# Performance work log

Hardware: AMD Instinct MI355X
Metric: run time of the kernel (lower is better)

The kernel has to match this reference:

```python
import jax, jax.numpy as jnp
import numpy as np

B, N, DIM = 4, 2048, 1024
HEADS, DHEAD = 16, 64
N_MEM = 64
INNER = HEADS * DHEAD  # 1024


def setup_inputs() -> dict:
    key = jax.random.key(0)
    ks = jax.random.split(key, 8)
    x = jax.random.normal(ks[0], (B, N, DIM), dtype=jnp.float32)
    memories = jax.random.normal(ks[1], (N_MEM, DIM), dtype=jnp.float32)
    attn_mask = jnp.ones((1, 1, N, N + N_MEM), dtype=bool)
    scale = 1.0 / np.sqrt(DIM)
    ln_gamma = jnp.ones((DIM,), dtype=jnp.float32)
    ln_beta = jnp.zeros((DIM,), dtype=jnp.float32)
    Wq = jax.random.normal(ks[2], (DIM, INNER), dtype=jnp.float32) * scale
    Wkv = jax.random.normal(ks[3], (DIM, 2 * INNER), dtype=jnp.float32) * scale
    Wo = jax.random.normal(ks[4], (INNER, DIM), dtype=jnp.float32) * scale
    bo = jnp.zeros((DIM,), dtype=jnp.float32)
    return {"x": x, "attn_mask": attn_mask, "memories": memories,
            "ln_gamma": ln_gamma, "ln_beta": ln_beta,
            "Wq": Wq, "Wkv": Wkv, "Wo": Wo, "bo": bo}


def _layernorm(x, gamma, beta, eps=1e-5):
    mu = jnp.mean(x, axis=-1, keepdims=True)
    var = jnp.var(x, axis=-1, keepdims=True)
    return (x - mu) * jax.lax.rsqrt(var + eps) * gamma + beta


def reference(x, attn_mask, memories, ln_gamma, ln_beta, Wq, Wkv, Wo, bo):
    b = x.shape[0]
    xn = _layernorm(x, ln_gamma, ln_beta)
    # memories: [n_mem, d] -> broadcast to [b, n_mem, d], concat on kv length
    mem = jnp.broadcast_to(memories[None], (b, memories.shape[0], memories.shape[1]))
    x_kv = jnp.concatenate([xn, mem], axis=1)  # [b, n+n_mem, d]
    q = xn @ Wq                                 # [b, n, inner]
    kv = x_kv @ Wkv                             # [b, nk, 2*inner]
    k, v = jnp.split(kv, 2, axis=-1)
    # split heads: b n (h d) -> b h n d
    def heads(t):
        bsz, n, _ = t.shape
        return t.reshape(bsz, n, HEADS, DHEAD).transpose(0, 2, 1, 3)
    q, k, v = heads(q), heads(k), heads(v)
    scale = DHEAD ** -0.5
    dots = jnp.einsum('bhnd,bhmd->bhnm', q, k) * scale  # [b,h,n,nk]
    neg = -jnp.finfo(dots.dtype).max
    dots = jnp.where(attn_mask, dots, neg)
    attn = jax.nn.softmax(dots, axis=-1)
    out = jnp.einsum('bhnm,bhmd->bhnd', attn, v)        # [b,h,n,d]
    out = out.transpose(0, 2, 1, 3).reshape(b, -1, INNER)
    return out @ Wo + bo
```

## Files before the change

kernel.cpp:

```cpp
#include <hip/hip_runtime.h>

using f16 = _Float16;
typedef _Float16 f16x8 __attribute__((ext_vector_type(8)));
typedef _Float16 f16x4 __attribute__((ext_vector_type(4)));
typedef float f32x4 __attribute__((ext_vector_type(4)));
typedef float f32x16 __attribute__((ext_vector_type(16)));
typedef uint32_t u32;
typedef unsigned int u32x4 __attribute__((ext_vector_type(4)));
typedef __fp16 h16x2 __attribute__((ext_vector_type(2)));

constexpr int DIMC   = 1024;
constexpr int NSEQ   = 2048;
constexpr int NKV    = 2112;
constexpr int NCHUNK = 33;
constexpr int NBATCH = 4;

__device__ __forceinline__ int swz8(int row, int slot) { return slot ^ (row & 7); }

__device__ __forceinline__ u32 pkrtz(float a, float b) {
    h16x2 t = __builtin_amdgcn_cvt_pkrtz(a, b);
    return __builtin_bit_cast(u32, t);
}

__device__ __forceinline__ void gld16(const f16* g, f16* l) {
    __builtin_amdgcn_global_load_lds(
        (const __attribute__((address_space(1))) u32*)g,
        (__attribute__((address_space(3))) u32*)l,
        16, 0, 0);
}

__global__ __launch_bounds__(256)
void ln_kernel(const float* __restrict__ x, const float* __restrict__ gamma,
               const float* __restrict__ beta, f16* __restrict__ xn)
{
    const int row = blockIdx.x;
    const int tid = threadIdx.x;
    const float4 v = *reinterpret_cast<const float4*>(x + (size_t)row * DIMC + tid * 4);
    float s  = v.x + v.y + v.z + v.w;
    float ss = v.x*v.x + v.y*v.y + v.z*v.z + v.w*v.w;
#pragma unroll
    for (int off = 1; off < 64; off <<= 1) {
        s  += __shfl_xor(s,  off, 64);
        ss += __shfl_xor(ss, off, 64);
    }
    __shared__ float ps[4], pss[4];
    const int w = tid >> 6;
    if ((tid & 63) == 0) { ps[w] = s; pss[w] = ss; }
    __syncthreads();
    s  = ps[0]  + ps[1]  + ps[2]  + ps[3];
    ss = pss[0] + pss[1] + pss[2] + pss[3];
    const float mu   = s * (1.0f / 1024.0f);
    const float var  = ss * (1.0f / 1024.0f) - mu * mu;
    const float rstd = rsqrtf(var + 1e-5f);
    const float4 gv = *reinterpret_cast<const float4*>(gamma + tid * 4);
    const float4 bv = *reinterpret_cast<const float4*>(beta  + tid * 4);
    f16x4 o;
    o[0] = (f16)((v.x - mu) * rstd * gv.x + bv.x);
    o[1] = (f16)((v.y - mu) * rstd * gv.y + bv.y);
    o[2] = (f16)((v.z - mu) * rstd * gv.z + bv.z);
    o[3] = (f16)((v.w - mu) * rstd * gv.w + bv.w);
    *reinterpret_cast<f16x4*>(xn + (size_t)row * DIMC + tid * 4) = o;
}

__global__ __launch_bounds__(256)
void transpose_cast(const float* __restrict__ in, f16* __restrict__ out,
                    int R, int C, float scale)
{
    __shared__ float tile[32][33];
    const int c0 = blockIdx.x * 32;
    const int r0 = blockIdx.y * 32;
    const int tx = threadIdx.x;
    const int ty = threadIdx.y;
#pragma unroll
    for (int i = 0; i < 4; ++i)
        tile[ty + i * 8][tx] = in[(size_t)(r0 + ty + i * 8) * C + c0 + tx];
    __syncthreads();
#pragma unroll
    for (int i = 0; i < 4; ++i)
        out[(size_t)(c0 + ty + i * 8) * R + r0 + tx] = (f16)(tile[tx][ty + i * 8] * scale);
}

__global__ __launch_bounds__(256)
void cast_kernel(const float* __restrict__ in, f16* __restrict__ out)
{
    const int i = blockIdx.x * 256 + threadIdx.x;
    const float4 v = *reinterpret_cast<const float4*>(in + (size_t)i * 4);
    f16x4 o; o[0] = (f16)v.x; o[1] = (f16)v.y; o[2] = (f16)v.z; o[3] = (f16)v.w;
    *reinterpret_cast<f16x4*>(out + (size_t)i * 4) = o;
}

template<int MODE>
__device__ __forceinline__ void gemm_body(
    int tm, int tn, f16* As, f16* Bs,
    const f16* __restrict__ A, const f16* __restrict__ BT,
    const f16* __restrict__ mem16,
    f16* __restrict__ Cf16, f16* __restrict__ Vt,
    float* __restrict__ Cf32, const float* __restrict__ bias)
{
    const int tid = threadIdx.x;
    const int lane = tid & 63, w = tid >> 6;
    const int wm = (w >> 1) * 64, wn = (w & 1) * 64;
    const int l3 = lane >> 3, l7 = lane & 7;
    const int gslot = (l7 ^ l3) * 8;

    f32x4 acc[4][4] = {};

    const f16* ag[4];
    const f16* bg[4];
#pragma unroll
    for (int i = 0; i < 4; ++i) {
        const int rl = w * 32 + i * 8 + l3;
        const int gm = tm * 128 + rl;
        if (MODE == 1) {
            const int bb = gm / NKV;
            const int rr = gm - bb * NKV;
            ag[i] = ((rr < NSEQ) ? (A + ((size_t)bb * NSEQ + rr) * DIMC)
                                 : (mem16 + (size_t)(rr - NSEQ) * DIMC)) + gslot;
        } else {
            ag[i] = A + (size_t)gm * DIMC + gslot;
        }
        bg[i] = BT + (size_t)(tn * 128 + rl) * DIMC + gslot;
    }

    for (int kt = 0; kt < DIMC; kt += 64) {
#pragma unroll
        for (int i = 0; i < 4; ++i) {
            gld16(ag[i] + kt, &As[(w * 32 + i * 8) * 64]);
            gld16(bg[i] + kt, &Bs[(w * 32 + i * 8) * 64]);
        }
        asm volatile("s_waitcnt vmcnt(0)" ::: "memory");
        __syncthreads();
#pragma unroll
        for (int kk = 0; kk < 2; ++kk) {
            f16x8 af[4], bf[4];
            const int rsel  = lane & 15;
            const int slot0 = (lane >> 4) + kk * 4;
#pragma unroll
            for (int mi = 0; mi < 4; ++mi) {
                const int row = wm + mi * 16 + rsel;
                af[mi] = *reinterpret_cast<const f16x8*>(&As[row * 64 + swz8(row, slot0) * 8]);
            }
#pragma unroll
            for (int nj = 0; nj < 4; ++nj) {
                const int row = wn + nj * 16 + rsel;
                bf[nj] = *reinterpret_cast<const f16x8*>(&Bs[row * 64 + swz8(row, slot0) * 8]);
            }
            __builtin_amdgcn_s_setprio(1);
#pragma unroll
            for (int mi = 0; mi < 4; ++mi)
#pragma unroll
                for (int nj = 0; nj < 4; ++nj)
                    acc[mi][nj] = __builtin_amdgcn_mfma_f32_16x16x32_f16(af[mi], bf[nj], acc[mi][nj], 0, 0, 0);
            __builtin_amdgcn_s_setprio(0);
        }
        __syncthreads();
    }

    const int cl = lane & 15, g = lane >> 4;
#pragma unroll
    for (int mi = 0; mi < 4; ++mi) {
#pragma unroll
        for (int nj = 0; nj < 4; ++nj) {
            const int col = tn * 128 + wn + nj * 16 + cl;
            if (MODE == 1 && col >= DIMC) {
                const int gm0 = tm * 128 + wm + mi * 16 + g * 4;
                const int bb = gm0 / NKV;
                const int rr = gm0 - bb * NKV;
                const int vc = col - DIMC;
                f16x4 pk;
                pk[0] = (f16)acc[mi][nj][0]; pk[1] = (f16)acc[mi][nj][1];
                pk[2] = (f16)acc[mi][nj][2]; pk[3] = (f16)acc[mi][nj][3];
                *reinterpret_cast<f16x4*>(
                    Vt + ((((size_t)bb * 16 + (vc >> 6)) * NCHUNK + (rr >> 6)) * 64 + (vc & 63)) * 64 + (rr & 63)) = pk;
            } else {
#pragma unroll
                for (int j = 0; j < 4; ++j) {
                    const int gm = tm * 128 + wm + mi * 16 + g * 4 + j;
                    const float val = acc[mi][nj][j];
                    if (MODE == 0) {
                        const int bb = gm >> 11, rr = gm & 2047;
                        Cf16[(((size_t)bb * 16 + (col >> 6)) * NSEQ + rr) * 64 + (col & 63)] = (f16)val;
                    } else if (MODE == 1) {
                        const int bb = gm / NKV;
                        const int rr = gm - bb * NKV;
                        Cf16[(((size_t)bb * 16 + (col >> 6)) * NKV + rr) * 64 + (col & 63)] = (f16)val;
                    } else {
                        Cf32[(size_t)gm * DIMC + col] = val + bias[col];
                    }
                }
            }
        }
    }
}

__global__ __launch_bounds__(256, 3)
void gemm_qkv(const f16* __restrict__ xn, const f16* __restrict__ wqT,
              const f16* __restrict__ wkvT, const f16* __restrict__ mem16,
              f16* __restrict__ q16, f16* __restrict__ k16, f16* __restrict__ vt16)
{
    __shared__ __align__(16) f16 As[128 * 64];
    __shared__ __align__(16) f16 Bs[128 * 64];
    if (blockIdx.y < 16) {
        gemm_body<1>(blockIdx.x, blockIdx.y, As, Bs, xn, wkvT, mem16, k16, vt16, nullptr, nullptr);
    } else {
        if (blockIdx.x >= 64) return;
        gemm_body<0>(blockIdx.x, blockIdx.y - 16, As, Bs, xn, wqT, nullptr, q16, nullptr, nullptr, nullptr);
    }
}

__global__ __launch_bounds__(256, 3)
void gemm_o(const f16* __restrict__ ao, const f16* __restrict__ woT,
            float* __restrict__ out, const float* __restrict__ bo)
{
    __shared__ __align__(16) f16 As[128 * 64];
    __shared__ __align__(16) f16 Bs[128 * 64];
    gemm_body<2>(blockIdx.x, blockIdx.y, As, Bs, ao, woT, nullptr, nullptr, nullptr, out, bo);
}

__global__ __launch_bounds__(256, 2)
void attn_kernel(const f16* __restrict__ q16, const f16* __restrict__ k16,
                 const f16* __restrict__ vt16, f16* __restrict__ ao16)
{
    __shared__ __align__(16) f16 Kb[4][64 * 64];
    __shared__ __align__(16) f16 Vb[4][64 * 64];

    const int raw = blockIdx.x;
    const int bh = (raw & 7) * 8 + ((raw >> 3) & 7);
    const int qt = raw >> 6;
    const int b = bh >> 4, h = bh & 15;
    const int tid = threadIdx.x, lane = tid & 63, w = tid >> 6;
    const int l31 = lane & 31, hi = lane >> 5;
    const int l3 = lane >> 3, l7 = lane & 7;
    const int gslot = (l7 ^ l3) * 8;

    const f16* kbase = k16  + (size_t)bh * NKV * 64;
    const f16* vbase = vt16 + (size_t)bh * NCHUNK * 4096;
    const f16* qbase = q16  + (size_t)bh * NSEQ * 64;

    const f16* kp[2];
    const f16* vp[2];
#pragma unroll
    for (int i = 0; i < 2; ++i) {
        const int off = (w * 16 + i * 8 + l3) * 64 + gslot;
        kp[i] = kbase + off;
        vp[i] = vbase + off;
    }

    f16x8 qf[2][4];
#pragma unroll
    for (int qb = 0; qb < 2; ++qb)
#pragma unroll
        for (int ks = 0; ks < 4; ++ks) {
            const int qrow = qt * 256 + w * 64 + qb * 32 + l31;
            qf[qb][ks] = *reinterpret_cast<const f16x8*>(
                qbase + (size_t)qrow * 64 + ks * 16 + hi * 8);
        }

    f32x16 Oa[2][2] = {};
    float lacc[2] = {0.0f, 0.0f};

#pragma unroll
    for (int c = 0; c < 3; ++c) {
#pragma unroll
        for (int i = 0; i < 2; ++i) {
            gld16(kp[i] + (size_t)c * 4096, &Kb[c][(w * 16 + i * 8) * 64]);
            gld16(vp[i] + (size_t)c * 4096, &Vb[c][(w * 16 + i * 8) * 64]);
        }
    }

    for (int t = 0; t < NCHUNK; ++t) {
        if (t <= 30)      asm volatile("s_waitcnt vmcnt(8)" ::: "memory");
        else if (t == 31) asm volatile("s_waitcnt vmcnt(4)" ::: "memory");
        else              asm volatile("s_waitcnt vmcnt(0)" ::: "memory");
        __builtin_amdgcn_s_barrier();

        if (t <= 29) {
            const int nb = (t + 3) & 3;
#pragma unroll
            for (int i = 0; i < 2; ++i) {
                gld16(kp[i] + (size_t)(t + 3) * 4096, &Kb[nb][(w * 16 + i * 8) * 64]);
                gld16(vp[i] + (size_t)(t + 3) * 4096, &Vb[nb][(w * 16 + i * 8) * 64]);
            }
        }
        const f16* Ks = Kb[t & 3];
        const f16* Vs = Vb[t & 3];

#pragma unroll
        for (int kb = 0; kb < 2; ++kb) {
            const int krow = kb * 32 + l31;
            f16x8 kf[4];
#pragma unroll
            for (int ks = 0; ks < 4; ++ks)
                kf[ks] = *reinterpret_cast<const f16x8*>(
                    &Ks[krow * 64 + ((2 * ks + hi) ^ (krow & 7)) * 8]);

            f32x16 sA = {}, sB = {};
            __builtin_amdgcn_s_setprio(1);
#pragma unroll
            for (int ks = 0; ks < 4; ++ks) {
                sA = __builtin_amdgcn_mfma_f32_32x32x16_f16(kf[ks], qf[0][ks], sA, 0, 0, 0);
                sB = __builtin_amdgcn_mfma_f32_32x32x16_f16(kf[ks], qf[1][ks], sB, 0, 0, 0);
            }
            __builtin_amdgcn_s_setprio(0);

            f16x8 pb[2][2];
#pragma unroll
            for (int qb = 0; qb < 2; ++qb) {
                const f32x16 sv = qb ? sB : sA;
                float p[16];
                float sum = 0.0f;
#pragma unroll
                for (int r = 0; r < 16; ++r) {
                    p[r] = __builtin_amdgcn_exp2f(sv[r] - 8.0f);
                    sum += p[r];
                }
                lacc[qb] += sum;
#pragma unroll
                for (int s2 = 0; s2 < 2; ++s2) {
                    u32 a  = pkrtz(p[s2 * 8 + 0], p[s2 * 8 + 1]);
                    u32 bb2 = pkrtz(p[s2 * 8 + 2], p[s2 * 8 + 3]);
                    u32 c  = pkrtz(p[s2 * 8 + 4], p[s2 * 8 + 5]);
                    u32 d  = pkrtz(p[s2 * 8 + 6], p[s2 * 8 + 7]);
                    asm volatile("v_permlane32_swap_b32 %0, %1" : "+v"(a),  "+v"(c));
                    asm volatile("v_permlane32_swap_b32 %0, %1" : "+v"(bb2), "+v"(d));
                    u32x4 wv = {a, bb2, c, d};
                    pb[qb][s2] = __builtin_bit_cast(f16x8, wv);
                }
            }

#pragma unroll
            for (int s2 = 0; s2 < 2; ++s2) {
                const int s = kb * 2 + s2;
                const int vr1 = 32 + l31;
                const f16x8 vf0 = *reinterpret_cast<const f16x8*>(
                    &Vs[l31 * 64 + ((2 * s + hi) ^ (l31 & 7)) * 8]);
                const f16x8 vf1 = *reinterpret_cast<const f16x8*>(
                    &Vs[vr1 * 64 + ((2 * s + hi) ^ (vr1 & 7)) * 8]);
                __builtin_amdgcn_s_setprio(1);
                Oa[0][0] = __builtin_amdgcn_mfma_f32_32x32x16_f16(vf0, pb[0][s2], Oa[0][0], 0, 0, 0);
                Oa[0][1] = __builtin_amdgcn_mfma_f32_32x32x16_f16(vf1, pb[0][s2], Oa[0][1], 0, 0, 0);
                Oa[1][0] = __builtin_amdgcn_mfma_f32_32x32x16_f16(vf0, pb[1][s2], Oa[1][0], 0, 0, 0);
                Oa[1][1] = __builtin_amdgcn_mfma_f32_32x32x16_f16(vf1, pb[1][s2], Oa[1][1], 0, 0, 0);
                __builtin_amdgcn_s_setprio(0);
            }
        }
        __builtin_amdgcn_s_barrier();
    }

#pragma unroll
    for (int qb = 0; qb < 2; ++qb) {
        const float l0 = lacc[qb] + __shfl_xor(lacc[qb], 32, 64);
        const float rinv = 1.0f / l0;
        const int qrow = qt * 256 + w * 64 + qb * 32 + l31;
#pragma unroll
        for (int db = 0; db < 2; ++db) {
#pragma unroll
            for (int rq = 0; rq < 4; ++rq) {
                const int d0 = db * 32 + rq * 8 + hi * 4;
                f16x4 pk;
                pk[0] = (f16)(Oa[qb][db][rq * 4 + 0] * rinv);
                pk[1] = (f16)(Oa[qb][db][rq * 4 + 1] * rinv);
                pk[2] = (f16)(Oa[qb][db][rq * 4 + 2] * rinv);
                pk[3] = (f16)(Oa[qb][db][rq * 4 + 3] * rinv);
                *reinterpret_cast<f16x4*>(
                    ao16 + ((size_t)(b * NSEQ + qrow)) * DIMC + h * 64 + d0) = pk;
            }
        }
    }
}

extern "C" void kernel_launch(void* const* d_in, const int* in_sizes, int n_in,
                              void* d_out, int out_size, void* d_ws, size_t ws_size,
                              hipStream_t stream)
{
    const float* x        = (const float*)d_in[0];
    const float* memories = (const float*)d_in[2];
    const float* ln_gamma = (const float*)d_in[3];
    const float* ln_beta  = (const float*)d_in[4];
    const float* Wq       = (const float*)d_in[5];
    const float* Wkv      = (const float*)d_in[6];
    const float* Wo       = (const float*)d_in[7];
    const float* bo       = (const float*)d_in[8];
    float* out = (float*)d_out;

    char* ws = (char*)d_ws;
    f16* xn16  = (f16*)(ws);
    f16* q16   = (f16*)(ws + (16ull << 20));
    f16* k16   = (f16*)(ws + (32ull << 20));
    f16* vt16  = (f16*)(ws + (49ull << 20));
    f16* wqT   = (f16*)(ws + (66ull << 20));
    f16* wkvT  = (f16*)(ws + (68ull << 20));
    f16* woT   = (f16*)(ws + (72ull << 20));
    f16* mem16 = (f16*)(ws + (74ull << 20));
    f16* ao16  = xn16;

    transpose_cast<<<dim3(32, 32), dim3(32, 8), 0, stream>>>(Wq,  wqT,  1024, 1024, 0.125f * 1.44269504088896341f);
    transpose_cast<<<dim3(64, 32), dim3(32, 8), 0, stream>>>(Wkv, wkvT, 1024, 2048, 1.0f);
    transpose_cast<<<dim3(32, 32), dim3(32, 8), 0, stream>>>(Wo,  woT,  1024, 1024, 1.0f);
    cast_kernel<<<64, 256, 0, stream>>>(memories, mem16);

    ln_kernel<<<NBATCH * NSEQ, 256, 0, stream>>>(x, ln_gamma, ln_beta, xn16);

    gemm_qkv<<<dim3(66, 24), 256, 0, stream>>>(xn16, wqT, wkvT, mem16, q16, k16, vt16);

    attn_kernel<<<dim3(512), 256, 0, stream>>>(q16, k16, vt16, ao16);

    gemm_o<<<dim3(64, 8), 256, 0, stream>>>(ao16, woT, out, bo);

    (void)in_sizes; (void)n_in; (void)out_size; (void)ws_size;
}
```

Baseline: 216.8 us.

## Split attention work across 8 waves with double-buffered K/V and fdot2 row sums

The attention kernel moves from 4 waves each owning 64 query rows to 8 waves each owning 32 rows, which halves per-wave accumulators and raises occupancy through launch bounds of 512 threads. The K/V LDS ring shrinks from a 4-deep prefetch to a 2-deep double buffer with a full vmcnt(0) wait every chunk. Row-sum accumulation now uses packed fp16 dot products on the already-rounded probabilities instead of fp32 adds. The trade is more latency hiding from extra waves against a shallower prefetch, less K fragment reuse per wave, and a softmax sum taken from fp16-rounded values.

```diff
diff --git a/kernel.cpp b/kernel.cpp
--- a/kernel.cpp
+++ b/kernel.cpp
@@ -217,12 +217,12 @@
     gemm_body<2>(blockIdx.x, blockIdx.y, As, Bs, ao, woT, nullptr, nullptr, nullptr, out, bo);
 }
 
-__global__ __launch_bounds__(256, 2)
+__global__ __launch_bounds__(512, 4)
 void attn_kernel(const f16* __restrict__ q16, const f16* __restrict__ k16,
                  const f16* __restrict__ vt16, f16* __restrict__ ao16)
 {
-    __shared__ __align__(16) f16 Kb[4][64 * 64];
-    __shared__ __align__(16) f16 Vb[4][64 * 64];
+    __shared__ __align__(16) f16 Kb[2][64 * 64];
+    __shared__ __align__(16) f16 Vb[2][64 * 64];
 
     const int raw = blockIdx.x;
     const int bh = (raw & 7) * 8 + ((raw >> 3) & 7);
@@ -237,53 +237,38 @@
     const f16* vbase = vt16 + (size_t)bh * NCHUNK * 4096;
     const f16* qbase = q16  + (size_t)bh * NSEQ * 64;
 
-    const f16* kp[2];
-    const f16* vp[2];
-#pragma unroll
-    for (int i = 0; i < 2; ++i) {
-        const int off = (w * 16 + i * 8 + l3) * 64 + gslot;
-        kp[i] = kbase + off;
-        vp[i] = vbase + off;
-    }
-
-    f16x8 qf[2][4];
-#pragma unroll
-    for (int qb = 0; qb < 2; ++qb)
-#pragma unroll
-        for (int ks = 0; ks < 4; ++ks) {
-            const int qrow = qt * 256 + w * 64 + qb * 32 + l31;
-            qf[qb][ks] = *reinterpret_cast<const f16x8*>(
+    const int srow = w * 8 + l3;
+    const f16* kp = kbase + (size_t)srow * 64 + gslot;
+    const f16* vp = vbase + (size_t)srow * 64 + gslot;
+
+    f16x8 qf[4];
+    {
+        const int qrow = qt * 256 + w * 32 + l31;
+#pragma unroll
+        for (int ks = 0; ks < 4; ++ks)
+            qf[ks] = *reinterpret_cast<const f16x8*>(
                 qbase + (size_t)qrow * 64 + ks * 16 + hi * 8);
-        }
-
-    f32x16 Oa[2][2] = {};
-    float lacc[2] = {0.0f, 0.0f};
-
-#pragma unroll
-    for (int c = 0; c < 3; ++c) {
-#pragma unroll
-        for (int i = 0; i < 2; ++i) {
-            gld16(kp[i] + (size_t)c * 4096, &Kb[c][(w * 16 + i * 8) * 64]);
-            gld16(vp[i] + (size_t)c * 4096, &Vb[c][(w * 16 + i * 8) * 64]);
-        }
-    }
+    }
+
+    f32x16 Oa0 = {}, Oa1 = {};
+    float lp0 = 0.0f, lp1 = 0.0f, lp2 = 0.0f, lp3 = 0.0f;
+
+    gld16(kp, &Kb[0][w * 8 * 64]);
+    gld16(vp, &Vb[0][w * 8 * 64]);
+
+#if __has_builtin(__builtin_amdgcn_fdot2)
+    const h16x2 ones = {(__fp16)1.0f, (__fp16)1.0f};
+#endif
 
     for (int t = 0; t < NCHUNK; ++t) {
-        if (t <= 30)      asm volatile("s_waitcnt vmcnt(8)" ::: "memory");
-        else if (t == 31) asm volatile("s_waitcnt vmcnt(4)" ::: "memory");
-        else              asm volatile("s_waitcnt vmcnt(0)" ::: "memory");
+        asm volatile("s_waitcnt vmcnt(0)" ::: "memory");
         __builtin_amdgcn_s_barrier();
-
-        if (t <= 29) {
-            const int nb = (t + 3) & 3;
-#pragma unroll
-            for (int i = 0; i < 2; ++i) {
-                gld16(kp[i] + (size_t)(t + 3) * 4096, &Kb[nb][(w * 16 + i * 8) * 64]);
-                gld16(vp[i] + (size_t)(t + 3) * 4096, &Vb[nb][(w * 16 + i * 8) * 64]);
-            }
-        }
-        const f16* Ks = Kb[t & 3];
-        const f16* Vs = Vb[t & 3];
+        if (t + 1 < NCHUNK) {
+            gld16(kp + (size_t)(t + 1) * 4096, &Kb[(t + 1) & 1][w * 8 * 64]);
+            gld16(vp + (size_t)(t + 1) * 4096, &Vb[(t + 1) & 1][w * 8 * 64]);
+        }
+        const f16* Ks = Kb[t & 1];
+        const f16* Vs = Vb[t & 1];
 
 #pragma unroll
         for (int kb = 0; kb < 2; ++kb) {
@@ -294,38 +279,44 @@
                 kf[ks] = *reinterpret_cast<const f16x8*>(
                     &Ks[krow * 64 + ((2 * ks + hi) ^ (krow & 7)) * 8]);
 
-            f32x16 sA = {}, sB = {};
+            f32x16 sA = {};
             __builtin_amdgcn_s_setprio(1);
 #pragma unroll
-            for (int ks = 0; ks < 4; ++ks) {
-                sA = __builtin_amdgcn_mfma_f32_32x32x16_f16(kf[ks], qf[0][ks], sA, 0, 0, 0);
-                sB = __builtin_amdgcn_mfma_f32_32x32x16_f16(kf[ks], qf[1][ks], sB, 0, 0, 0);
-            }
+            for (int ks = 0; ks < 4; ++ks)
+                sA = __builtin_amdgcn_mfma_f32_32x32x16_f16(kf[ks], qf[ks], sA, 0, 0, 0);
             __builtin_amdgcn_s_setprio(0);
 
-            f16x8 pb[2][2];
-#pragma unroll
-            for (int qb = 0; qb < 2; ++qb) {
-                const f32x16 sv = qb ? sB : sA;
-                float p[16];
-                float sum = 0.0f;
-#pragma unroll
-                for (int r = 0; r < 16; ++r) {
-                    p[r] = __builtin_amdgcn_exp2f(sv[r] - 8.0f);
-                    sum += p[r];
+            float p[16];
+#pragma unroll
+            for (int r = 0; r < 16; ++r)
+                p[r] = __builtin_amdgcn_exp2f(sA[r] - 8.0f);
+
+            f16x8 pb[2];
+#pragma unroll
+            for (int s2 = 0; s2 < 2; ++s2) {
+                u32 a  = pkrtz(p[s2 * 8 + 0], p[s2 * 8 + 1]);
+                u32 b2 = pkrtz(p[s2 * 8 + 2], p[s2 * 8 + 3]);
+                u32 c  = pkrtz(p[s2 * 8 + 4], p[s2 * 8 + 5]);
+                u32 d  = pkrtz(p[s2 * 8 + 6], p[s2 * 8 + 7]);
+                asm volatile("v_permlane32_swap_b32 %0, %1" : "+v"(a),  "+v"(c));
+                asm volatile("v_permlane32_swap_b32 %0, %1" : "+v"(b2), "+v"(d));
+#if __has_builtin(__builtin_amdgcn_fdot2)
+                lp0 = __builtin_amdgcn_fdot2(__builtin_bit_cast(h16x2, a),  ones, lp0, false);
+                lp1 = __builtin_amdgcn_fdot2(__builtin_bit_cast(h16x2, b2), ones, lp1, false);
+                lp2 = __builtin_amdgcn_fdot2(__builtin_bit_cast(h16x2, c),  ones, lp2, false);
+                lp3 = __builtin_amdgcn_fdot2(__builtin_bit_cast(h16x2, d),  ones, lp3, false);
+#else
+                {
+                    h16x2 ha = __builtin_bit_cast(h16x2, a),  hb = __builtin_bit_cast(h16x2, b2);
+                    h16x2 hc = __builtin_bit_cast(h16x2, c),  hd = __builtin_bit_cast(h16x2, d);
+                    lp0 += (float)ha[0] + (float)ha[1];
+                    lp1 += (float)hb[0] + (float)hb[1];
+                    lp2 += (float)hc[0] + (float)hc[1];
+                    lp3 += (float)hd[0] + (float)hd[1];
                 }
-                lacc[qb] += sum;
-#pragma unroll
-                for (int s2 = 0; s2 < 2; ++s2) {
-                    u32 a  = pkrtz(p[s2 * 8 + 0], p[s2 * 8 + 1]);
-                    u32 bb2 = pkrtz(p[s2 * 8 + 2], p[s2 * 8 + 3]);
-                    u32 c  = pkrtz(p[s2 * 8 + 4], p[s2 * 8 + 5]);
-                    u32 d  = pkrtz(p[s2 * 8 + 6], p[s2 * 8 + 7]);
-                    asm volatile("v_permlane32_swap_b32 %0, %1" : "+v"(a),  "+v"(c));
-                    asm volatile("v_permlane32_swap_b32 %0, %1" : "+v"(bb2), "+v"(d));
-                    u32x4 wv = {a, bb2, c, d};
-                    pb[qb][s2] = __builtin_bit_cast(f16x8, wv);
-                }
+#endif
+                u32x4 wv = {a, b2, c, d};
+                pb[s2] = __builtin_bit_cast(f16x8, wv);
             }
 
 #pragma unroll
@@ -337,35 +328,38 @@
                 const f16x8 vf1 = *reinterpret_cast<const f16x8*>(
                     &Vs[vr1 * 64 + ((2 * s + hi) ^ (vr1 & 7)) * 8]);
                 __builtin_amdgcn_s_setprio(1);
-                Oa[0][0] = __builtin_amdgcn_mfma_f32_32x32x16_f16(vf0, pb[0][s2], Oa[0][0], 0, 0, 0);
-                Oa[0][1] = __builtin_amdgcn_mfma_f32_32x32x16_f16(vf1, pb[0][s2], Oa[0][1], 0, 0, 0);
-                Oa[1][0] = __builtin_amdgcn_mfma_f32_32x32x16_f16(vf0, pb[1][s2], Oa[1][0], 0, 0, 0);
-                Oa[1][1] = __builtin_amdgcn_mfma_f32_32x32x16_f16(vf1, pb[1][s2], Oa[1][1], 0, 0, 0);
+                Oa0 = __builtin_amdgcn_mfma_f32_32x32x16_f16(vf0, pb[s2], Oa0, 0, 0, 0);
+                Oa1 = __builtin_amdgcn_mfma_f32_32x32x16_f16(vf1, pb[s2], Oa1, 0, 0, 0);
                 __builtin_amdgcn_s_setprio(0);
             }
         }
-        __builtin_amdgcn_s_barrier();
-    }
-
-#pragma unroll
-    for (int qb = 0; qb < 2; ++qb) {
-        const float l0 = lacc[qb] + __shfl_xor(lacc[qb], 32, 64);
-        const float rinv = 1.0f / l0;
-        const int qrow = qt * 256 + w * 64 + qb * 32 + l31;
-#pragma unroll
-        for (int db = 0; db < 2; ++db) {
-#pragma unroll
-            for (int rq = 0; rq < 4; ++rq) {
-                const int d0 = db * 32 + rq * 8 + hi * 4;
-                f16x4 pk;
-                pk[0] = (f16)(Oa[qb][db][rq * 4 + 0] * rinv);
-                pk[1] = (f16)(Oa[qb][db][rq * 4 + 1] * rinv);
-                pk[2] = (f16)(Oa[qb][db][rq * 4 + 2] * rinv);
-                pk[3] = (f16)(Oa[qb][db][rq * 4 + 3] * rinv);
-                *reinterpret_cast<f16x4*>(
-                    ao16 + ((size_t)(b * NSEQ + qrow)) * DIMC + h * 64 + d0) = pk;
-            }
-        }
+    }
+
+    float l0 = (lp0 + lp1) + (lp2 + lp3);
+    l0 += __shfl_xor(l0, 32, 64);
+    const float rinv = 1.0f / l0;
+    const int qrow = qt * 256 + w * 32 + l31;
+#pragma unroll
+    for (int rq = 0; rq < 4; ++rq) {
+        const int d0 = rq * 8 + hi * 4;
+        f16x4 pk;
+        pk[0] = (f16)(Oa0[rq * 4 + 0] * rinv);
+        pk[1] = (f16)(Oa0[rq * 4 + 1] * rinv);
+        pk[2] = (f16)(Oa0[rq * 4 + 2] * rinv);
+        pk[3] = (f16)(Oa0[rq * 4 + 3] * rinv);
+        *reinterpret_cast<f16x4*>(
+            ao16 + ((size_t)(b * NSEQ + qrow)) * DIMC + h * 64 + d0) = pk;
+    }
+#pragma unroll
+    for (int rq = 0; rq < 4; ++rq) {
+        const int d0 = 32 + rq * 8 + hi * 4;
+        f16x4 pk;
+        pk[0] = (f16)(Oa1[rq * 4 + 0] * rinv);
+        pk[1] = (f16)(Oa1[rq * 4 + 1] * rinv);
+        pk[2] = (f16)(Oa1[rq * 4 + 2] * rinv);
+        pk[3] = (f16)(Oa1[rq * 4 + 3] * rinv);
+        *reinterpret_cast<f16x4*>(
+            ao16 + ((size_t)(b * NSEQ + qrow)) * DIMC + h * 64 + d0) = pk;
     }
 }
 
@@ -403,7 +397,7 @@
 
     gemm_qkv<<<dim3(66, 24), 256, 0, stream>>>(xn16, wqT, wkvT, mem16, q16, k16, vt16);
 
-    attn_kernel<<<dim3(512), 256, 0, stream>>>(q16, k16, vt16, ao16);
+    attn_kernel<<<dim3(512), 512, 0, stream>>>(q16, k16, vt16, ao16);
 
     gemm_o<<<dim3(64, 8), 256, 0, stream>>>(ao16, woT, out, bo);
 
```

Result: faster. 208.8 us (-3.7%).

## Double attention block to 8 waves, restructure chunk loop and use fdot2 row sums

Applied to the files above, without the earlier changes.

The attention kernel now runs 512 threads per block, so each block covers 512 query rows over 256 blocks and every K/V chunk staged in shared memory is reused by twice as many waves. Each wave loads one 8-row slice per chunk, and the chunk loop is manually unrolled by four with fixed buffer indices and waitcnts. The QK, softmax and PV steps are interleaved per query block to lower register pressure. Row sums are accumulated from the packed fp16 probabilities with fdot2 instead of fp32 adds. The cost is only 256 blocks to fill the GPU, and the sums are now taken on fp16-rounded values.

```diff
diff --git a/kernel.cpp b/kernel.cpp
--- a/kernel.cpp
+++ b/kernel.cpp
@@ -217,7 +217,7 @@
     gemm_body<2>(blockIdx.x, blockIdx.y, As, Bs, ao, woT, nullptr, nullptr, nullptr, out, bo);
 }
 
-__global__ __launch_bounds__(256, 2)
+__global__ __launch_bounds__(512, 2)
 void attn_kernel(const f16* __restrict__ q16, const f16* __restrict__ k16,
                  const f16* __restrict__ vt16, f16* __restrict__ ao16)
 {
@@ -232,126 +232,138 @@
     const int l31 = lane & 31, hi = lane >> 5;
     const int l3 = lane >> 3, l7 = lane & 7;
     const int gslot = (l7 ^ l3) * 8;
+    const int x7 = l31 & 7;
 
     const f16* kbase = k16  + (size_t)bh * NKV * 64;
     const f16* vbase = vt16 + (size_t)bh * NCHUNK * 4096;
     const f16* qbase = q16  + (size_t)bh * NSEQ * 64;
 
-    const f16* kp[2];
-    const f16* vp[2];
-#pragma unroll
-    for (int i = 0; i < 2; ++i) {
-        const int off = (w * 16 + i * 8 + l3) * 64 + gslot;
-        kp[i] = kbase + off;
-        vp[i] = vbase + off;
-    }
+    const int srow = w * 8 + l3;
+    const f16* kp = kbase + (size_t)srow * 64 + gslot;
+    const f16* vp = vbase + (size_t)srow * 64 + gslot;
 
     f16x8 qf[2][4];
 #pragma unroll
     for (int qb = 0; qb < 2; ++qb)
 #pragma unroll
         for (int ks = 0; ks < 4; ++ks) {
-            const int qrow = qt * 256 + w * 64 + qb * 32 + l31;
+            const int qrow = qt * 512 + w * 64 + qb * 32 + l31;
             qf[qb][ks] = *reinterpret_cast<const f16x8*>(
                 qbase + (size_t)qrow * 64 + ks * 16 + hi * 8);
         }
 
     f32x16 Oa[2][2] = {};
-    float lacc[2] = {0.0f, 0.0f};
+    float lp[2] = {0.0f, 0.0f};
 
 #pragma unroll
     for (int c = 0; c < 3; ++c) {
-#pragma unroll
-        for (int i = 0; i < 2; ++i) {
-            gld16(kp[i] + (size_t)c * 4096, &Kb[c][(w * 16 + i * 8) * 64]);
-            gld16(vp[i] + (size_t)c * 4096, &Vb[c][(w * 16 + i * 8) * 64]);
-        }
-    }
-
-    for (int t = 0; t < NCHUNK; ++t) {
-        if (t <= 30)      asm volatile("s_waitcnt vmcnt(8)" ::: "memory");
-        else if (t == 31) asm volatile("s_waitcnt vmcnt(4)" ::: "memory");
-        else              asm volatile("s_waitcnt vmcnt(0)" ::: "memory");
-        __builtin_amdgcn_s_barrier();
-
-        if (t <= 29) {
-            const int nb = (t + 3) & 3;
-#pragma unroll
-            for (int i = 0; i < 2; ++i) {
-                gld16(kp[i] + (size_t)(t + 3) * 4096, &Kb[nb][(w * 16 + i * 8) * 64]);
-                gld16(vp[i] + (size_t)(t + 3) * 4096, &Vb[nb][(w * 16 + i * 8) * 64]);
-            }
-        }
-        const f16* Ks = Kb[t & 3];
-        const f16* Vs = Vb[t & 3];
-
+        gld16(kp + (size_t)c * 4096, &Kb[c][w * 8 * 64]);
+        gld16(vp + (size_t)c * 4096, &Vb[c][w * 8 * 64]);
+    }
+
+#if __has_builtin(__builtin_amdgcn_fdot2)
+    const h16x2 ones = {(__fp16)1.0f, (__fp16)1.0f};
+#endif
+
+    auto compute = [&](const f16* __restrict__ Ks, const f16* __restrict__ Vs) {
 #pragma unroll
         for (int kb = 0; kb < 2; ++kb) {
-            const int krow = kb * 32 + l31;
             f16x8 kf[4];
 #pragma unroll
             for (int ks = 0; ks < 4; ++ks)
                 kf[ks] = *reinterpret_cast<const f16x8*>(
-                    &Ks[krow * 64 + ((2 * ks + hi) ^ (krow & 7)) * 8]);
-
-            f32x16 sA = {}, sB = {};
-            __builtin_amdgcn_s_setprio(1);
-#pragma unroll
-            for (int ks = 0; ks < 4; ++ks) {
-                sA = __builtin_amdgcn_mfma_f32_32x32x16_f16(kf[ks], qf[0][ks], sA, 0, 0, 0);
-                sB = __builtin_amdgcn_mfma_f32_32x32x16_f16(kf[ks], qf[1][ks], sB, 0, 0, 0);
-            }
-            __builtin_amdgcn_s_setprio(0);
-
-            f16x8 pb[2][2];
+                    &Ks[(kb * 32 + l31) * 64 + ((2 * ks + hi) ^ x7) * 8]);
+            f16x8 vf[2][2];
+#pragma unroll
+            for (int db = 0; db < 2; ++db)
+#pragma unroll
+                for (int s2 = 0; s2 < 2; ++s2)
+                    vf[db][s2] = *reinterpret_cast<const f16x8*>(
+                        &Vs[(db * 32 + l31) * 64 + ((2 * (kb * 2 + s2) + hi) ^ x7) * 8]);
+
 #pragma unroll
             for (int qb = 0; qb < 2; ++qb) {
-                const f32x16 sv = qb ? sB : sA;
-                float p[16];
-                float sum = 0.0f;
-#pragma unroll
-                for (int r = 0; r < 16; ++r) {
-                    p[r] = __builtin_amdgcn_exp2f(sv[r] - 8.0f);
-                    sum += p[r];
+                f32x16 sv = {};
+                __builtin_amdgcn_s_setprio(1);
+#pragma unroll
+                for (int ks = 0; ks < 4; ++ks)
+                    sv = __builtin_amdgcn_mfma_f32_32x32x16_f16(kf[ks], qf[qb][ks], sv, 0, 0, 0);
+                __builtin_amdgcn_s_setprio(0);
+
+                f16x8 pb[2];
+#pragma unroll
+                for (int s2 = 0; s2 < 2; ++s2) {
+                    const float p0 = __builtin_amdgcn_exp2f(sv[s2 * 8 + 0] - 8.0f);
+                    const float p1 = __builtin_amdgcn_exp2f(sv[s2 * 8 + 1] - 8.0f);
+                    const float p2 = __builtin_amdgcn_exp2f(sv[s2 * 8 + 2] - 8.0f);
+                    const float p3 = __builtin_amdgcn_exp2f(sv[s2 * 8 + 3] - 8.0f);
+                    const float p4 = __builtin_amdgcn_exp2f(sv[s2 * 8 + 4] - 8.0f);
+                    const float p5 = __builtin_amdgcn_exp2f(sv[s2 * 8 + 5] - 8.0f);
+                    const float p6 = __builtin_amdgcn_exp2f(sv[s2 * 8 + 6] - 8.0f);
+                    const float p7 = __builtin_amdgcn_exp2f(sv[s2 * 8 + 7] - 8.0f);
+                    u32 a  = pkrtz(p0, p1);
+                    u32 b2 = pkrtz(p2, p3);
+                    u32 c  = pkrtz(p4, p5);
+                    u32 d  = pkrtz(p6, p7);
+                    asm volatile("v_permlane32_swap_b32 %0, %1" : "+v"(a),  "+v"(c));
+                    asm volatile("v_permlane32_swap_b32 %0, %1" : "+v"(b2), "+v"(d));
+#if __has_builtin(__builtin_amdgcn_fdot2)
+                    lp[qb] = __builtin_amdgcn_fdot2(__builtin_bit_cast(h16x2, a),  ones, lp[qb], false);
+                    lp[qb] = __builtin_amdgcn_fdot2(__builtin_bit_cast(h16x2, b2), ones, lp[qb], false);
+                    lp[qb] = __builtin_amdgcn_fdot2(__builtin_bit_cast(h16x2, c),  ones, lp[qb], false);
+                    lp[qb] = __builtin_amdgcn_fdot2(__builtin_bit_cast(h16x2, d),  ones, lp[qb], false);
+#else
+                    {
+                        h16x2 ha = __builtin_bit_cast(h16x2, a),  hb = __builtin_bit_cast(h16x2, b2);
+                        h16x2 hc = __builtin_bit_cast(h16x2, c),  hd = __builtin_bit_cast(h16x2, d);
+                        lp[qb] += (float)ha[0] + (float)ha[1] + (float)hb[0] + (float)hb[1]
+                                + (float)hc[0] + (float)hc[1] + (float)hd[0] + (float)hd[1];
+                    }
+#endif
+                    u32x4 wv = {a, b2, c, d};
+                    pb[s2] = __builtin_bit_cast(f16x8, wv);
                 }
-                lacc[qb] += sum;
+
+                __builtin_amdgcn_s_setprio(1);
 #pragma unroll
                 for (int s2 = 0; s2 < 2; ++s2) {
-                    u32 a  = pkrtz(p[s2 * 8 + 0], p[s2 * 8 + 1]);
-                    u32 bb2 = pkrtz(p[s2 * 8 + 2], p[s2 * 8 + 3]);
-                    u32 c  = pkrtz(p[s2 * 8 + 4], p[s2 * 8 + 5]);
-                    u32 d  = pkrtz(p[s2 * 8 + 6], p[s2 * 8 + 7]);
-                    asm volatile("v_permlane32_swap_b32 %0, %1" : "+v"(a),  "+v"(c));
-                    asm volatile("v_permlane32_swap_b32 %0, %1" : "+v"(bb2), "+v"(d));
-                    u32x4 wv = {a, bb2, c, d};
-                    pb[qb][s2] = __builtin_bit_cast(f16x8, wv);
+                    Oa[qb][0] = __builtin_amdgcn_mfma_f32_32x32x16_f16(vf[0][s2], pb[s2], Oa[qb][0], 0, 0, 0);
+                    Oa[qb][1] = __builtin_amdgcn_mfma_f32_32x32x16_f16(vf[1][s2], pb[s2], Oa[qb][1], 0, 0, 0);
                 }
-            }
-
-#pragma unroll
-            for (int s2 = 0; s2 < 2; ++s2) {
-                const int s = kb * 2 + s2;
-                const int vr1 = 32 + l31;
-                const f16x8 vf0 = *reinterpret_cast<const f16x8*>(
-                    &Vs[l31 * 64 + ((2 * s + hi) ^ (l31 & 7)) * 8]);
-                const f16x8 vf1 = *reinterpret_cast<const f16x8*>(
-                    &Vs[vr1 * 64 + ((2 * s + hi) ^ (vr1 & 7)) * 8]);
-                __builtin_amdgcn_s_setprio(1);
-                Oa[0][0] = __builtin_amdgcn_mfma_f32_32x32x16_f16(vf0, pb[0][s2], Oa[0][0], 0, 0, 0);
-                Oa[0][1] = __builtin_amdgcn_mfma_f32_32x32x16_f16(vf1, pb[0][s2], Oa[0][1], 0, 0, 0);
-                Oa[1][0] = __builtin_amdgcn_mfma_f32_32x32x16_f16(vf0, pb[1][s2], Oa[1][0], 0, 0, 0);
-                Oa[1][1] = __builtin_amdgcn_mfma_f32_32x32x16_f16(vf1, pb[1][s2], Oa[1][1], 0, 0, 0);
                 __builtin_amdgcn_s_setprio(0);
             }
         }
-        __builtin_amdgcn_s_barrier();
-    }
+    };
+
+#define CHUNK(T, CB, NB, W, PF)                                               \
+    do {                                                                      \
+        asm volatile("s_waitcnt vmcnt(" #W ")" ::: "memory");                 \
+        __builtin_amdgcn_s_barrier();                                         \
+        if (PF) {                                                             \
+            gld16(kp + (size_t)((T) + 3) * 4096, &Kb[NB][w * 8 * 64]);        \
+            gld16(vp + (size_t)((T) + 3) * 4096, &Vb[NB][w * 8 * 64]);        \
+        }                                                                     \
+        compute(&Kb[CB][0], &Vb[CB][0]);                                      \
+    } while (0)
+
+    for (int t0 = 0; t0 < 28; t0 += 4) {
+        CHUNK(t0 + 0, 0, 3, 4, true);
+        CHUNK(t0 + 1, 1, 0, 4, true);
+        CHUNK(t0 + 2, 2, 1, 4, true);
+        CHUNK(t0 + 3, 3, 2, 4, true);
+    }
+    CHUNK(28, 0, 3, 4, true);
+    CHUNK(29, 1, 0, 4, true);
+    CHUNK(30, 2, 1, 4, false);
+    CHUNK(31, 3, 3, 2, false);
+    CHUNK(32, 0, 0, 0, false);
+#undef CHUNK
 
 #pragma unroll
     for (int qb = 0; qb < 2; ++qb) {
-        const float l0 = lacc[qb] + __shfl_xor(lacc[qb], 32, 64);
+        float l0 = lp[qb] + __shfl_xor(lp[qb], 32, 64);
         const float rinv = 1.0f / l0;
-        const int qrow = qt * 256 + w * 64 + qb * 32 + l31;
+        const int qrow = qt * 512 + w * 64 + qb * 32 + l31;
 #pragma unroll
         for (int db = 0; db < 2; ++db) {
 #pragma unroll
@@ -403,7 +415,7 @@
 
     gemm_qkv<<<dim3(66, 24), 256, 0, stream>>>(xn16, wqT, wkvT, mem16, q16, k16, vt16);
 
-    attn_kernel<<<dim3(512), 256, 0, stream>>>(q16, k16, vt16, ao16);
+    attn_kernel<<<dim3(256), 512, 0, stream>>>(q16, k16, vt16, ao16);
 
     gemm_o<<<dim3(64, 8), 256, 0, stream>>>(ao16, woT, out, bo);
 
```

Result: faster. 212.2 us (-2.1%).
